# Performance work log

Hardware: AMD Instinct MI355X
Metric: run time of the kernel (lower is better)

The kernel has to match this reference:

```python
import jax, jax.numpy as jnp
import numpy as np

NEG_SLOPE = 0.2


def setup_inputs() -> dict:
    key = jax.random.key(0)
    ks = jax.random.split(key, 7)
    N, E, F_IN, H, D = 100000, 1600000, 256, 4, 64
    feat = jax.random.normal(ks[0], (N, F_IN), dtype=jnp.float32)
    W = jax.random.normal(ks[1], (F_IN, H * D), dtype=jnp.float32) * (1.0 / np.sqrt(F_IN))
    attn_l = jax.random.normal(ks[2], (H, D), dtype=jnp.float32) * 0.1
    attn_r = jax.random.normal(ks[3], (H, D), dtype=jnp.float32) * 0.1
    bias = jnp.zeros((H * D,), dtype=jnp.float32)
    src = jax.random.randint(ks[4], (E,), 0, N, dtype=jnp.int32)
    dst = jax.random.randint(ks[5], (E,), 0, N, dtype=jnp.int32)
    return {"feat": feat, "W": W, "attn_l": attn_l, "attn_r": attn_r,
            "bias": bias, "src": src, "dst": dst}


def reference(feat, W, attn_l, attn_r, bias, src, dst):
    N = feat.shape[0]
    H, D = attn_l.shape
    # fc: [N, F_in] @ [F_in, H*D] -> [N, H, D]
    h = (feat @ W).reshape(N, H, D)
    # per-node attention logits (dot with attn vectors): [N, H]
    el = jnp.einsum('nhd,hd->nh', h, attn_l)
    er = jnp.einsum('nhd,hd->nh', h, attn_r)
    # edge scores: e_ij = LeakyReLU(el[src] + er[dst]) -> [E, H]
    e = el[src] + er[dst]
    e = jnp.where(e > 0, e, NEG_SLOPE * e)
    # segment softmax over destination neighborhoods
    e_max = jax.ops.segment_max(e, dst, num_segments=N)          # [N, H]
    e_max = jnp.where(jnp.isfinite(e_max), e_max, 0.0)           # guard 0-in-degree
    e_exp = jnp.exp(e - e_max[dst])                              # [E, H]
    denom = jax.ops.segment_sum(e_exp, dst, num_segments=N)      # [N, H]
    a = e_exp / jnp.maximum(denom[dst], 1e-16)                   # [E, H]
    # weighted scatter-add of source messages: [E, H, D] -> [N, H, D]
    msg = h[src] * a[:, :, None]
    out = jax.ops.segment_sum(msg, dst, num_segments=N)
    out = out + bias.reshape(1, H, D)
    return out
```

## Files before the change

### kernel.cpp

```cpp
#include <hip/hip_runtime.h>
#include <hip/hip_bf16.h>
#include <math.h>

#define HEADS 4
#define DHEAD 64
#define HD 256
#define F_IN 256
#define NEG_SLOPE 0.2f

typedef __attribute__((ext_vector_type(8))) short bf16x8;
typedef __attribute__((ext_vector_type(8))) ushort u16x8;
typedef __attribute__((ext_vector_type(4))) float f32x4;

__device__ __forceinline__ ushort f2bf(float f) {
    __hip_bfloat16 b = __float2bfloat16(f);
    ushort u; __builtin_memcpy(&u, &b, 2);
    return u;
}

__global__ __launch_bounds__(256) void wtcast_k(const float* __restrict__ W,
                                                ushort* __restrict__ Wt) {
    int i = blockIdx.x * 256 + threadIdx.x;
    int k = i >> 8, c = i & 255;
    int ct = c >> 4, kb = k >> 5, kh = (k >> 3) & 3, j = k & 7;
    int l = kh * 16 + (c & 15);
    Wt[(size_t)((ct * 8 + kb) * 64 + l) * 8 + j] = f2bf(W[i]);
}

#define HIST_BLOCKS 2048
__global__ __launch_bounds__(256) void fused_k(const float* __restrict__ A,
                                               const ushort* __restrict__ Wt,
                                               const float* __restrict__ attn_l,
                                               const float* __restrict__ attn_r,
                                               ushort* __restrict__ hbf,
                                               float* __restrict__ el,
                                               float* __restrict__ er,
                                               const int* __restrict__ dst,
                                               int* __restrict__ counts,
                                               ushort* __restrict__ pos,
                                               int M, int E, int GB) {
    __shared__ ushort As[64 * 256];

    if (blockIdx.x >= GB) {
        const int stride = HIST_BLOCKS * 256;
        for (int i = (blockIdx.x - GB) * 256 + threadIdx.x; i < E; i += stride)
            pos[i] = (ushort)atomicAdd(&counts[dst[i]], 1);
        return;
    }

    const int tid = threadIdx.x;
    const int wave = tid >> 6;
    const int lane = tid & 63;
    const int r16 = lane & 15;
    const int khalf = lane >> 4;
    const int row0 = blockIdx.x * 64;
    const int wcol0 = wave * 64;

    bf16x8 b[4][8];
#pragma unroll
    for (int nc = 0; nc < 4; ++nc) {
        const int ct = wave * 4 + nc;
#pragma unroll
        for (int kb = 0; kb < 8; ++kb)
            b[nc][kb] = *(const bf16x8*)(Wt + ((size_t)(ct * 8 + kb) * 64 + lane) * 8);
    }

    {
        const int srow = tid >> 2;
        const int cg = tid & 3;
        int arow = row0 + srow; if (arow >= M) arow = M - 1;
        const float* ap = A + (size_t)arow * F_IN + cg * 64;
        const int sw = (srow & 7) << 4;
        char* wb = (char*)As + srow * 512;
#pragma unroll
        for (int q = 0; q < 8; ++q) {
            float4 f0 = *(const float4*)(ap + q * 8);
            float4 f1 = *(const float4*)(ap + q * 8 + 4);
            u16x8 cv;
            cv[0] = f2bf(f0.x); cv[1] = f2bf(f0.y); cv[2] = f2bf(f0.z); cv[3] = f2bf(f0.w);
            cv[4] = f2bf(f1.x); cv[5] = f2bf(f1.y); cv[6] = f2bf(f1.z); cv[7] = f2bf(f1.w);
            *(u16x8*)(wb + ((cg * 128 + q * 16) ^ sw)) = cv;
        }
    }
    __syncthreads();

    f32x4 acc[4][4] = {};
#pragma unroll
    for (int kb = 0; kb < 8; ++kb) {
        bf16x8 a[4];
#pragma unroll
        for (int mr = 0; mr < 4; ++mr) {
            const int row = mr * 16 + r16;
            const int sw = (row & 7) << 4;
            a[mr] = *(const bf16x8*)((const char*)As + row * 512 +
                                     ((kb * 64 + khalf * 16) ^ sw));
        }
#pragma unroll
        for (int mr = 0; mr < 4; ++mr)
#pragma unroll
            for (int nc = 0; nc < 4; ++nc)
                acc[mr][nc] = __builtin_amdgcn_mfma_f32_16x16x32_bf16(
                    a[mr], b[nc][kb], acc[mr][nc], 0, 0, 0);
    }

    float al[4], ar[4];
#pragma unroll
    for (int nc = 0; nc < 4; ++nc) {
        al[nc] = attn_l[wcol0 + nc * 16 + r16];
        ar[nc] = attn_r[wcol0 + nc * 16 + r16];
    }
#pragma unroll
    for (int mr = 0; mr < 4; ++mr) {
#pragma unroll
        for (int r = 0; r < 4; ++r) {
            int row = row0 + mr * 16 + khalf * 4 + r;
            float vl = 0.f, vr = 0.f;
#pragma unroll
            for (int nc = 0; nc < 4; ++nc) {
                float v = acc[mr][nc][r];
                vl = fmaf(v, al[nc], vl);
                vr = fmaf(v, ar[nc], vr);
            }
#pragma unroll
            for (int off = 1; off < 16; off <<= 1) {
                vl += __shfl_xor(vl, off);
                vr += __shfl_xor(vr, off);
            }
            if (row < M) {
                if (r16 == 0) {
                    el[row * HEADS + wave] = vl;
                    er[row * HEADS + wave] = vr;
                }
#pragma unroll
                for (int nc = 0; nc < 4; ++nc)
                    hbf[(size_t)row * HD + wcol0 + nc * 16 + r16] = f2bf(acc[mr][nc][r]);
            }
        }
    }
}

#define SCAN_SPAN 4096
__global__ __launch_bounds__(1024) void blocksum_k(const int* __restrict__ counts,
                                                   int* __restrict__ btot, int N) {
    __shared__ int wsum[16];
    const int tid = threadIdx.x, lane = tid & 63, wid = tid >> 6;
    int i0 = blockIdx.x * SCAN_SPAN + tid * 4;
    int t = 0;
#pragma unroll
    for (int r = 0; r < 4; ++r) { int i = i0 + r; if (i < N) t += counts[i]; }
#pragma unroll
    for (int off = 32; off; off >>= 1) t += __shfl_xor(t, off);
    if (lane == 0) wsum[wid] = t;
    __syncthreads();
    if (tid == 0) {
        int s = 0;
        for (int w = 0; w < 16; ++w) s += wsum[w];
        btot[blockIdx.x] = s;
    }
}

__global__ __launch_bounds__(64) void scanb_k(const int* __restrict__ btot,
                                              int* __restrict__ boff, int nb) {
    int lane = threadIdx.x;
    int v = (lane < nb) ? btot[lane] : 0;
    int sc = v;
    for (int off = 1; off < 64; off <<= 1) {
        int u = __shfl_up(sc, off);
        if (lane >= off) sc += u;
    }
    if (lane < nb) boff[lane] = sc - v;
}

__global__ __launch_bounds__(1024) void scanw_k(const int* __restrict__ counts,
                                                const int* __restrict__ boff,
                                                int* __restrict__ row_start, int N) {
    __shared__ int wsum[16];
    const int tid = threadIdx.x, lane = tid & 63, wid = tid >> 6;
    int i0 = blockIdx.x * SCAN_SPAN + tid * 4;
    int v[4]; int t = 0;
#pragma unroll
    for (int r = 0; r < 4; ++r) { int i = i0 + r; v[r] = (i < N) ? counts[i] : 0; t += v[r]; }
    int sc = t;
    for (int off = 1; off < 64; off <<= 1) {
        int u = __shfl_up(sc, off);
        if (lane >= off) sc += u;
    }
    if (lane == 63) wsum[wid] = sc;
    __syncthreads();
    int wpref = 0;
    for (int w = 0; w < wid; ++w) wpref += wsum[w];
    int excl = boff[blockIdx.x] + wpref + sc - t;
    int run = 0;
#pragma unroll
    for (int r = 0; r < 4; ++r) {
        int i = i0 + r;
        if (i < N) row_start[i] = excl + run;
        run += v[r];
    }
    if (N - 1 >= i0 && N - 1 < i0 + 4) row_start[N] = excl + run;
}

__global__ __launch_bounds__(256) void place_k(const int* __restrict__ src,
                                               const int* __restrict__ dst,
                                               const ushort* __restrict__ pos,
                                               const int* __restrict__ row_start,
                                               int* __restrict__ sorted_src, int E) {
    int i = blockIdx.x * 256 + threadIdx.x;
    if (i < E)
        sorted_src[row_start[dst[i]] + (int)pos[i]] = src[i];
}

__global__ __launch_bounds__(256) void gat4_k(const ushort* __restrict__ hbf,
                                              const float* __restrict__ el,
                                              const float* __restrict__ er,
                                              const float* __restrict__ bias,
                                              const int* __restrict__ row_start,
                                              const int* __restrict__ sorted_src,
                                              float* __restrict__ out, int N) {
    __shared__ int   s_idx[4][64];
    __shared__ float p_s[4][64][4];
    const int wv = threadIdx.x >> 6, lane = threadIdx.x & 63;
    const int head = lane >> 4;
    const int n = blockIdx.x * 4 + wv;
    if (n >= N) return;

    const int start = row_start[n], end = row_start[n + 1];
    const int deg = end - start;

    const float4 er4 = *(const float4*)&er[n * 4];
    const ushort* __restrict__ hrow = hbf + (unsigned)lane * 4u;

    float acc0 = 0.f, acc1 = 0.f, acc2 = 0.f, acc3 = 0.f, ssum = 0.f;

#define GLOAD(i, V, Q) { int s_ = s_idx[wv][i]; Q = p_s[wv][i][head]; \
                         V = *(const uint2*)(hrow + (size_t)(unsigned)s_ * HD); }
#define GUSE(V, Q) { union { unsigned u; float f; } b0_, b1_, b2_, b3_; \
                     b0_.u = V.x << 16; b1_.u = V.x & 0xffff0000u; \
                     b2_.u = V.y << 16; b3_.u = V.y & 0xffff0000u; \
                     acc0 = fmaf(Q, b0_.f, acc0); acc1 = fmaf(Q, b1_.f, acc1); \
                     acc2 = fmaf(Q, b2_.f, acc2); acc3 = fmaf(Q, b3_.f, acc3); \
                     ssum += Q; }

    for (int c0 = 0; c0 < deg; c0 += 64) {
        const int cnt = min(64, deg - c0);
        if (lane < cnt) {
            int s = sorted_src[start + c0 + lane];
            float4 e4 = *(const float4*)&el[s * 4];
            float4 pv;
            float x0 = e4.x + er4.x; x0 = fmaxf(x0, NEG_SLOPE * x0);
            float x1 = e4.y + er4.y; x1 = fmaxf(x1, NEG_SLOPE * x1);
            float x2 = e4.z + er4.z; x2 = fmaxf(x2, NEG_SLOPE * x2);
            float x3 = e4.w + er4.w; x3 = fmaxf(x3, NEG_SLOPE * x3);
            pv.x = __expf(x0); pv.y = __expf(x1); pv.z = __expf(x2); pv.w = __expf(x3);
            s_idx[wv][lane] = s;
            *(float4*)&p_s[wv][lane][0] = pv;
        }
        __builtin_amdgcn_wave_barrier();

        int k = 0;
        if (cnt >= 8) {
            uint2 va, vb, vc, vd; float qa, qb, qc, qd;
            GLOAD(0, va, qa); GLOAD(1, vb, qb); GLOAD(2, vc, qc); GLOAD(3, vd, qd);
            for (; k + 8 <= cnt; k += 4) {
                GUSE(va, qa); GLOAD(k + 4, va, qa);
                GUSE(vb, qb); GLOAD(k + 5, vb, qb);
                GUSE(vc, qc); GLOAD(k + 6, vc, qc);
                GUSE(vd, qd); GLOAD(k + 7, vd, qd);
            }
            GUSE(va, qa); GUSE(vb, qb); GUSE(vc, qc); GUSE(vd, qd);
            k += 4;
        }
        for (; k < cnt; ++k) { uint2 v; float q; GLOAD(k, v, q); GUSE(v, q); }
        __builtin_amdgcn_wave_barrier();
    }
#undef GLOAD
#undef GUSE

    const float inv = 1.0f / fmaxf(ssum, 1e-16f);
    const float4 b4 = *(const float4*)&bias[lane * 4];
    float4 o;
    o.x = fmaf(acc0, inv, b4.x);
    o.y = fmaf(acc1, inv, b4.y);
    o.z = fmaf(acc2, inv, b4.z);
    o.w = fmaf(acc3, inv, b4.w);
    *(float4*)&out[(size_t)n * HD + lane * 4] = o;
}

extern "C" void kernel_launch(void* const* d_in, const int* in_sizes, int n_in,
                              void* d_out, int out_size, void* d_ws, size_t ws_size,
                              hipStream_t stream) {
    const float* feat   = (const float*)d_in[0];
    const float* W      = (const float*)d_in[1];
    const float* attn_l = (const float*)d_in[2];
    const float* attn_r = (const float*)d_in[3];
    const float* bias   = (const float*)d_in[4];
    const int*   src    = (const int*)d_in[5];
    const int*   dst    = (const int*)d_in[6];

    const int N = in_sizes[0] / F_IN;
    const int E = in_sizes[5];

    ushort* hbf = (ushort*)d_ws;
    float* el = (float*)(hbf + (size_t)N * HD);
    float* er = el + (size_t)N * HEADS;
    int* counts     = (int*)(er + (size_t)N * HEADS);
    int* row_start  = counts + N;
    int* sorted_src = row_start + (N + 1);
    int* btot       = sorted_src + E;
    int* boff       = btot + 64;
    ushort* pos     = (ushort*)(boff + 64);
    ushort* Wt = (ushort*)(((uintptr_t)(pos + E) + 15) & ~(uintptr_t)15);

    float* out = (float*)d_out;

    const int nb = (N + SCAN_SPAN - 1) / SCAN_SPAN;
    const int GB = (N + 63) / 64;

    hipMemsetAsync(counts, 0, (size_t)N * sizeof(int), stream);
    wtcast_k<<<256, 256, 0, stream>>>(W, Wt);
    fused_k<<<GB + HIST_BLOCKS, 256, 0, stream>>>(feat, Wt, attn_l, attn_r,
                                                  hbf, el, er, dst, counts, pos, N, E, GB);

    blocksum_k<<<nb, 1024, 0, stream>>>(counts, btot, N);
    scanb_k<<<1, 64, 0, stream>>>(btot, boff, nb);
    scanw_k<<<nb, 1024, 0, stream>>>(counts, boff, row_start, N);
    place_k<<<(E + 255) / 256, 256, 0, stream>>>(src, dst, pos, row_start, sorted_src, E);

    gat4_k<<<(N + 3) / 4, 256, 0, stream>>>(hbf, el, er, bias, row_start, sorted_src, out, N);
}
```

Before: 297.4 us.

## Precompute edge exp-scores in placement kernel and fold memset into weight cast

Moves the LeakyReLU and exp edge-score computation from the aggregation kernel into the CSR placement kernel. There it is computed in edge order and stored as fp16 next to the sorted source index. The aggregation kernel then loads contiguous fp16 scores instead of doing a dependent gather of el per source. The counts memset is also merged into the weight-cast kernel, saving one launch. In exchange it adds an E*4 fp16 write and read, and fp16 storage of the unnormalised exp may lose precision or overflow for large logits.

Result: slower. 343.6 us (+15.5%).

```diff
diff --git a/kernel.cpp b/kernel.cpp
--- a/kernel.cpp
+++ b/kernel.cpp
@@ -17,14 +17,29 @@
     ushort u; __builtin_memcpy(&u, &b, 2);
     return u;
 }
-
-__global__ __launch_bounds__(256) void wtcast_k(const float* __restrict__ W,
-                                                ushort* __restrict__ Wt) {
-    int i = blockIdx.x * 256 + threadIdx.x;
-    int k = i >> 8, c = i & 255;
-    int ct = c >> 4, kb = k >> 5, kh = (k >> 3) & 3, j = k & 7;
-    int l = kh * 16 + (c & 15);
-    Wt[(size_t)((ct * 8 + kb) * 64 + l) * 8 + j] = f2bf(W[i]);
+__device__ __forceinline__ ushort f2h(float f) {
+    _Float16 h = (_Float16)f;
+    ushort u; __builtin_memcpy(&u, &h, 2);
+    return u;
+}
+__device__ __forceinline__ float h2f(ushort u) {
+    _Float16 h; __builtin_memcpy(&h, &u, 2);
+    return (float)h;
+}
+
+__global__ __launch_bounds__(256) void prep0_k(const float* __restrict__ W,
+                                               ushort* __restrict__ Wt,
+                                               int* __restrict__ counts, int N) {
+    if (blockIdx.x < 256) {
+        int i = blockIdx.x * 256 + threadIdx.x;
+        int k = i >> 8, c = i & 255;
+        int ct = c >> 4, kb = k >> 5, kh = (k >> 3) & 3, j = k & 7;
+        int l = kh * 16 + (c & 15);
+        Wt[(size_t)((ct * 8 + kb) * 64 + l) * 8 + j] = f2bf(W[i]);
+    } else {
+        int i = (blockIdx.x - 256) * 256 + threadIdx.x;
+        if (i < N) counts[i] = 0;
+    }
 }
 
 #define HIST_BLOCKS 2048
@@ -200,19 +215,34 @@
     if (N - 1 >= i0 && N - 1 < i0 + 4) row_start[N] = excl + run;
 }
 
-__global__ __launch_bounds__(256) void place_k(const int* __restrict__ src,
-                                               const int* __restrict__ dst,
-                                               const ushort* __restrict__ pos,
-                                               const int* __restrict__ row_start,
-                                               int* __restrict__ sorted_src, int E) {
+__global__ __launch_bounds__(256) void place2_k(const int* __restrict__ src,
+                                                const int* __restrict__ dst,
+                                                const ushort* __restrict__ pos,
+                                                const int* __restrict__ row_start,
+                                                const float* __restrict__ el,
+                                                const float* __restrict__ er,
+                                                int* __restrict__ sorted_src,
+                                                ushort* __restrict__ sorted_p,
+                                                int E) {
     int i = blockIdx.x * 256 + threadIdx.x;
-    if (i < E)
-        sorted_src[row_start[dst[i]] + (int)pos[i]] = src[i];
+    if (i >= E) return;
+    int s = src[i], d = dst[i];
+    int slot = row_start[d] + (int)pos[i];
+    float4 e4 = *(const float4*)&el[s * 4];
+    float4 r4 = *(const float4*)&er[d * 4];
+    float x0 = e4.x + r4.x; x0 = fmaxf(x0, NEG_SLOPE * x0);
+    float x1 = e4.y + r4.y; x1 = fmaxf(x1, NEG_SLOPE * x1);
+    float x2 = e4.z + r4.z; x2 = fmaxf(x2, NEG_SLOPE * x2);
+    float x3 = e4.w + r4.w; x3 = fmaxf(x3, NEG_SLOPE * x3);
+    ushort4 h;
+    h.x = f2h(__expf(x0)); h.y = f2h(__expf(x1));
+    h.z = f2h(__expf(x2)); h.w = f2h(__expf(x3));
+    sorted_src[slot] = s;
+    *(ushort4*)&sorted_p[(size_t)slot * 4] = h;
 }
 
 __global__ __launch_bounds__(256) void gat4_k(const ushort* __restrict__ hbf,
-                                              const float* __restrict__ el,
-                                              const float* __restrict__ er,
+                                              const ushort* __restrict__ sorted_p,
                                               const float* __restrict__ bias,
                                               const int* __restrict__ row_start,
                                               const int* __restrict__ sorted_src,
@@ -227,7 +257,6 @@
     const int start = row_start[n], end = row_start[n + 1];
     const int deg = end - start;
 
-    const float4 er4 = *(const float4*)&er[n * 4];
     const ushort* __restrict__ hrow = hbf + (unsigned)lane * 4u;
 
     float acc0 = 0.f, acc1 = 0.f, acc2 = 0.f, acc3 = 0.f, ssum = 0.f;
@@ -244,14 +273,11 @@
     for (int c0 = 0; c0 < deg; c0 += 64) {
         const int cnt = min(64, deg - c0);
         if (lane < cnt) {
-            int s = sorted_src[start + c0 + lane];
-            float4 e4 = *(const float4*)&el[s * 4];
+            int j = start + c0 + lane;
+            int s = sorted_src[j];
+            ushort4 hp = *(const ushort4*)&sorted_p[(size_t)j * 4];
             float4 pv;
-            float x0 = e4.x + er4.x; x0 = fmaxf(x0, NEG_SLOPE * x0);
-            float x1 = e4.y + er4.y; x1 = fmaxf(x1, NEG_SLOPE * x1);
-            float x2 = e4.z + er4.z; x2 = fmaxf(x2, NEG_SLOPE * x2);
-            float x3 = e4.w + er4.w; x3 = fmaxf(x3, NEG_SLOPE * x3);
-            pv.x = __expf(x0); pv.y = __expf(x1); pv.z = __expf(x2); pv.w = __expf(x3);
+            pv.x = h2f(hp.x); pv.y = h2f(hp.y); pv.z = h2f(hp.z); pv.w = h2f(hp.w);
             s_idx[wv][lane] = s;
             *(float4*)&p_s[wv][lane][0] = pv;
         }
@@ -309,22 +335,23 @@
     int* btot       = sorted_src + E;
     int* boff       = btot + 64;
     ushort* pos     = (ushort*)(boff + 64);
-    ushort* Wt = (ushort*)(((uintptr_t)(pos + E) + 15) & ~(uintptr_t)15);
+    ushort* sorted_p = pos + E;
+    ushort* Wt = (ushort*)(((uintptr_t)(sorted_p + (size_t)E * 4) + 15) & ~(uintptr_t)15);
 
     float* out = (float*)d_out;
 
     const int nb = (N + SCAN_SPAN - 1) / SCAN_SPAN;
     const int GB = (N + 63) / 64;
 
-    hipMemsetAsync(counts, 0, (size_t)N * sizeof(int), stream);
-    wtcast_k<<<256, 256, 0, stream>>>(W, Wt);
+    prep0_k<<<256 + (N + 255) / 256, 256, 0, stream>>>(W, Wt, counts, N);
     fused_k<<<GB + HIST_BLOCKS, 256, 0, stream>>>(feat, Wt, attn_l, attn_r,
                                                   hbf, el, er, dst, counts, pos, N, E, GB);
 
     blocksum_k<<<nb, 1024, 0, stream>>>(counts, btot, N);
     scanb_k<<<1, 64, 0, stream>>>(btot, boff, nb);
     scanw_k<<<nb, 1024, 0, stream>>>(counts, boff, row_start, N);
-    place_k<<<(E + 255) / 256, 256, 0, stream>>>(src, dst, pos, row_start, sorted_src, E);
-
-    gat4_k<<<(N + 3) / 4, 256, 0, stream>>>(hbf, el, er, bias, row_start, sorted_src, out, N);
-}
+    place2_k<<<(E + 255) / 256, 256, 0, stream>>>(src, dst, pos, row_start, el, er,
+                                                  sorted_src, sorted_p, E);
+
+    gat4_k<<<(N + 3) / 4, 256, 0, stream>>>(hbf, sorted_p, bias, row_start, sorted_src, out, N);
+}
```

## Give each wave full-width 16-row GEMM tiles loading A directly, dropping LDS staging

Applied to the files above, without the earlier changes.

The fused GEMM now has each wave compute 16 rows across all 256 output columns. The wave loads its A fragments straight from global memory into registers, so the shared-memory tile and barrier are gone. W fragments are streamed from global/L2 per k-step instead of being held in registers. This removes LDS traffic and synchronisation, but each wave now reads all of W, which raises L2 traffic and register pressure from the 16 accumulators.

Result: slower. 316.2 us (+6.3%).

```diff
diff --git a/kernel.cpp b/kernel.cpp
--- a/kernel.cpp
+++ b/kernel.cpp
@@ -39,8 +39,6 @@
                                                int* __restrict__ counts,
                                                ushort* __restrict__ pos,
                                                int M, int E, int GB) {
-    __shared__ ushort As[64 * 256];
-
     if (blockIdx.x >= GB) {
         const int stride = HIST_BLOCKS * 256;
         for (int i = (blockIdx.x - GB) * 256 + threadIdx.x; i < E; i += stride)
@@ -53,88 +51,65 @@
     const int lane = tid & 63;
     const int r16 = lane & 15;
     const int khalf = lane >> 4;
-    const int row0 = blockIdx.x * 64;
-    const int wcol0 = wave * 64;
-
-    bf16x8 b[4][8];
-#pragma unroll
-    for (int nc = 0; nc < 4; ++nc) {
-        const int ct = wave * 4 + nc;
-#pragma unroll
-        for (int kb = 0; kb < 8; ++kb)
-            b[nc][kb] = *(const bf16x8*)(Wt + ((size_t)(ct * 8 + kb) * 64 + lane) * 8);
-    }
-
-    {
-        const int srow = tid >> 2;
-        const int cg = tid & 3;
-        int arow = row0 + srow; if (arow >= M) arow = M - 1;
-        const float* ap = A + (size_t)arow * F_IN + cg * 64;
-        const int sw = (srow & 7) << 4;
-        char* wb = (char*)As + srow * 512;
-#pragma unroll
-        for (int q = 0; q < 8; ++q) {
-            float4 f0 = *(const float4*)(ap + q * 8);
-            float4 f1 = *(const float4*)(ap + q * 8 + 4);
-            u16x8 cv;
-            cv[0] = f2bf(f0.x); cv[1] = f2bf(f0.y); cv[2] = f2bf(f0.z); cv[3] = f2bf(f0.w);
-            cv[4] = f2bf(f1.x); cv[5] = f2bf(f1.y); cv[6] = f2bf(f1.z); cv[7] = f2bf(f1.w);
-            *(u16x8*)(wb + ((cg * 128 + q * 16) ^ sw)) = cv;
+    const int rowb = blockIdx.x * 64 + wave * 16;
+
+    int arow = rowb + r16; if (arow >= M) arow = M - 1;
+    const float* ap = A + (size_t)arow * F_IN + khalf * 8;
+
+    f32x4 acc[16] = {};
+
+#pragma unroll
+    for (int kb = 0; kb < 8; ++kb) {
+        float4 f0 = *(const float4*)(ap + kb * 32);
+        float4 f1 = *(const float4*)(ap + kb * 32 + 4);
+        union { u16x8 u; bf16x8 h; } cv;
+        cv.u[0] = f2bf(f0.x); cv.u[1] = f2bf(f0.y); cv.u[2] = f2bf(f0.z); cv.u[3] = f2bf(f0.w);
+        cv.u[4] = f2bf(f1.x); cv.u[5] = f2bf(f1.y); cv.u[6] = f2bf(f1.z); cv.u[7] = f2bf(f1.w);
+        bf16x8 a = cv.h;
+#pragma unroll
+        for (int ct = 0; ct < 16; ++ct) {
+            bf16x8 b = *(const bf16x8*)(Wt + ((size_t)(ct * 8 + kb) * 64 + lane) * 8);
+            acc[ct] = __builtin_amdgcn_mfma_f32_16x16x32_bf16(a, b, acc[ct], 0, 0, 0);
         }
     }
-    __syncthreads();
-
-    f32x4 acc[4][4] = {};
-#pragma unroll
-    for (int kb = 0; kb < 8; ++kb) {
-        bf16x8 a[4];
-#pragma unroll
-        for (int mr = 0; mr < 4; ++mr) {
-            const int row = mr * 16 + r16;
-            const int sw = (row & 7) << 4;
-            a[mr] = *(const bf16x8*)((const char*)As + row * 512 +
-                                     ((kb * 64 + khalf * 16) ^ sw));
-        }
-#pragma unroll
-        for (int mr = 0; mr < 4; ++mr)
-#pragma unroll
-            for (int nc = 0; nc < 4; ++nc)
-                acc[mr][nc] = __builtin_amdgcn_mfma_f32_16x16x32_bf16(
-                    a[mr], b[nc][kb], acc[mr][nc], 0, 0, 0);
-    }
-
-    float al[4], ar[4];
-#pragma unroll
-    for (int nc = 0; nc < 4; ++nc) {
-        al[nc] = attn_l[wcol0 + nc * 16 + r16];
-        ar[nc] = attn_r[wcol0 + nc * 16 + r16];
-    }
-#pragma unroll
-    for (int mr = 0; mr < 4; ++mr) {
-#pragma unroll
-        for (int r = 0; r < 4; ++r) {
-            int row = row0 + mr * 16 + khalf * 4 + r;
-            float vl = 0.f, vr = 0.f;
-#pragma unroll
-            for (int nc = 0; nc < 4; ++nc) {
-                float v = acc[mr][nc][r];
-                vl = fmaf(v, al[nc], vl);
-                vr = fmaf(v, ar[nc], vr);
+
+    float al[16], ar[16];
+#pragma unroll
+    for (int ct = 0; ct < 16; ++ct) {
+        al[ct] = attn_l[ct * 16 + r16];
+        ar[ct] = attn_r[ct * 16 + r16];
+    }
+#pragma unroll
+    for (int r = 0; r < 4; ++r) {
+        int row = rowb + khalf * 4 + r;
+        float vl[4] = {0.f, 0.f, 0.f, 0.f}, vr[4] = {0.f, 0.f, 0.f, 0.f};
+#pragma unroll
+        for (int h = 0; h < 4; ++h)
+#pragma unroll
+            for (int q = 0; q < 4; ++q) {
+                int ct = h * 4 + q;
+                float v = acc[ct][r];
+                vl[h] = fmaf(v, al[ct], vl[h]);
+                vr[h] = fmaf(v, ar[ct], vr[h]);
             }
 #pragma unroll
-            for (int off = 1; off < 16; off <<= 1) {
-                vl += __shfl_xor(vl, off);
-                vr += __shfl_xor(vr, off);
+        for (int off = 1; off < 16; off <<= 1)
+#pragma unroll
+            for (int h = 0; h < 4; ++h) {
+                vl[h] += __shfl_xor(vl[h], off);
+                vr[h] += __shfl_xor(vr[h], off);
             }
-            if (row < M) {
-                if (r16 == 0) {
-                    el[row * HEADS + wave] = vl;
-                    er[row * HEADS + wave] = vr;
+        if (row < M) {
+            if (r16 == 0) {
+#pragma unroll
+                for (int h = 0; h < 4; ++h) {
+                    el[row * HEADS + h] = vl[h];
+                    er[row * HEADS + h] = vr[h];
                 }
-#pragma unroll
-                for (int nc = 0; nc < 4; ++nc)
-                    hbf[(size_t)row * HD + wcol0 + nc * 16 + r16] = f2bf(acc[mr][nc][r]);
             }
+#pragma unroll
+            for (int ct = 0; ct < 16; ++ct)
+                hbf[(size_t)row * HD + ct * 16 + r16] = f2bf(acc[ct][r]);
         }
     }
 }
```
